# Performance work log

Hardware: AMD Instinct MI355X
Metric: run time of the kernel (lower is better)

Reference implementation:

```python
import jax, jax.numpy as jnp
import numpy as np


def setup_inputs() -> dict:
    key = jax.random.key(0)
    ks = jax.random.split(key, 8)
    n_src, n_dst, n_edges = 100000, 50000, 600000
    d_in, d_out = 128, 128
    n_reuse, n_cache = 5000, 8000
    full_dst_len = n_dst + n_reuse

    feat_src = jax.random.normal(ks[0], (n_src, d_in), jnp.float32)
    src = jax.random.randint(ks[1], (n_edges,), 0, n_src)
    dst = jax.random.randint(ks[2], (n_edges,), 0, n_dst)
    # xavier-ish init for the two bias-free Linear layers (stored as [out, in] like torch)
    W_self = jax.random.normal(ks[3], (d_out, d_in), jnp.float32) / np.sqrt(d_in).astype(np.float32)
    W_neigh = jax.random.normal(ks[4], (d_out, d_in), jnp.float32) / np.sqrt(d_in).astype(np.float32)
    # reuse_indices must be unique positions within [0, full_dst_len)
    reuse_indices = jnp.sort(jax.random.permutation(ks[5], full_dst_len)[:n_reuse])
    reuse_embedding = jax.random.normal(ks[6], (n_reuse, d_out), jnp.float32)
    cache_indices = jax.random.randint(ks[7], (n_cache,), 0, full_dst_len)
    return dict(feat_src=feat_src, W_self=W_self, W_neigh=W_neigh,
                reuse_embedding=reuse_embedding, src=src, dst=dst,
                reuse_indices=reuse_indices, cache_indices=cache_indices,
                n_dst=n_dst)


def reference(feat_src, W_self, W_neigh, reuse_embedding, src, dst,
              reuse_indices, cache_indices, n_dst):
    # --- GraphSAGE 'mean' aggregation on a block graph ---
    feat_dst = feat_src[:n_dst]                         # [n_dst, D_in]
    msgs = feat_src[src]                                # [E, D_in] copy_src gather
    ssum = jax.ops.segment_sum(msgs, dst, num_segments=n_dst)          # [n_dst, D_in]
    deg = jax.ops.segment_sum(jnp.ones_like(msgs[:, 0]), dst, num_segments=n_dst)
    h_neigh = jnp.where(deg[:, None] > 0, ssum / jnp.maximum(deg, 1.0)[:, None], 0.0)
    rst = feat_dst @ W_self.T + h_neigh @ W_neigh.T     # fc_self + fc_neigh

    # --- cache-reuse scatter merge (flag == 0 path) ---
    n_reuse = reuse_indices.shape[0]
    full_dst_len = n_dst + n_reuse
    keep = jnp.ones((full_dst_len,), dtype=bool).at[reuse_indices].set(False)
    unprune_indices = jnp.nonzero(keep, size=n_dst)[0]  # np.delete equivalent
    full = jnp.zeros((full_dst_len, rst.shape[1]), rst.dtype)
    full = full.at[unprune_indices].set(rst).at[reuse_indices].set(reuse_embedding)
    cache_embedding = jax.lax.stop_gradient(full[cache_indices])  # .detach()
    return full, cache_embedding
```

## Files before the change

kernel.cpp:

```cpp
#include <hip/hip_runtime.h>

#define N_DST   50000
#define D       128
#define MAXDEG  64

typedef __attribute__((ext_vector_type(8))) short bf16x8;
typedef __attribute__((ext_vector_type(4))) float f32x4;

__device__ __forceinline__ unsigned short f2bf(float f) {
    unsigned u = __float_as_uint(f);
    u += 0x7FFFu + ((u >> 16) & 1u);
    return (unsigned short)(u >> 16);
}

__global__ void build_ell_kernel(const int* __restrict__ src,
                                 const int* __restrict__ dst,
                                 int* __restrict__ ell,
                                 int* __restrict__ cnt,
                                 int n_edges) {
    int e = blockIdx.x * blockDim.x + threadIdx.x;
    if (e >= n_edges) return;
    int d = dst[e];
    int pos = atomicAdd(&cnt[d], 1);
    if (pos < MAXDEG)
        ell[(size_t)d * MAXDEG + pos] = src[e];
}

__global__ void rowpos_kernel(const int* __restrict__ reuse_idx,
                              int* __restrict__ rowpos, int n_reuse) {
    int i = blockIdx.x * blockDim.x + threadIdx.x;
    if (i >= N_DST) return;
    int lo = 0, hi = n_reuse;
    while (lo < hi) {
        int mid = (lo + hi) >> 1;
        if (reuse_idx[mid] - mid > i) hi = mid; else lo = mid + 1;
    }
    rowpos[i] = i + lo;
}

__global__ void wconv_kernel(const float* __restrict__ Wself,
                             const float* __restrict__ Wneigh,
                             unsigned short* __restrict__ wbf) {
    int idx = blockIdx.x * blockDim.x + threadIdx.x;
    if (idx >= 128 * 256) return;
    int n = idx >> 8;
    int k = idx & 255;
    float v = (k < 128) ? Wself[n * 128 + k] : Wneigh[n * 128 + (k - 128)];
    wbf[idx] = f2bf(v);
}

__global__ __launch_bounds__(256)
void gather_kernel(const float* __restrict__ feat,
                   const int* __restrict__ ell,
                   const int* __restrict__ cnt,
                   unsigned int* __restrict__ hneigh_u32) {
    int gid  = blockIdx.x * blockDim.x + threadIdx.x;
    int row  = gid >> 5;
    int lane = gid & 31;
    if (row >= N_DST) return;

    int deg = cnt[row];
    int n = min(deg, MAXDEG);
    float inv = 1.0f / fmaxf((float)deg, 1.0f);
    const int* rell = ell + (size_t)row * MAXDEG;

    float4 acc = make_float4(0.f, 0.f, 0.f, 0.f);
    int j = 0;
    for (; j + 4 <= n; j += 4) {
        int s0 = rell[j + 0];
        int s1 = rell[j + 1];
        int s2 = rell[j + 2];
        int s3 = rell[j + 3];
        float4 v0 = *(const float4*)&feat[(size_t)s0 * D + 4 * lane];
        float4 v1 = *(const float4*)&feat[(size_t)s1 * D + 4 * lane];
        float4 v2 = *(const float4*)&feat[(size_t)s2 * D + 4 * lane];
        float4 v3 = *(const float4*)&feat[(size_t)s3 * D + 4 * lane];
        acc.x += v0.x + v1.x + v2.x + v3.x;
        acc.y += v0.y + v1.y + v2.y + v3.y;
        acc.z += v0.z + v1.z + v2.z + v3.z;
        acc.w += v0.w + v1.w + v2.w + v3.w;
    }
    for (; j < n; ++j) {
        int s = rell[j];
        float4 v = *(const float4*)&feat[(size_t)s * D + 4 * lane];
        acc.x += v.x;
        acc.y += v.y;
        acc.z += v.z;
        acc.w += v.w;
    }
    unsigned p0 = (unsigned)f2bf(acc.x * inv) | ((unsigned)f2bf(acc.y * inv) << 16);
    unsigned p1 = (unsigned)f2bf(acc.z * inv) | ((unsigned)f2bf(acc.w * inv) << 16);
    uint2 out; out.x = p0; out.y = p1;
    *(uint2*)&hneigh_u32[(size_t)row * 64 + 2 * lane] = out;
}

__global__ __launch_bounds__(256, 2)
void gemm_kernel(const float* __restrict__ feat,
                 const unsigned short* __restrict__ hneigh,
                 const unsigned short* __restrict__ wbf,
                 const int* __restrict__ rowpos,
                 float* __restrict__ full) {
    __shared__ unsigned short Wl[128 * 256];

    int tid = threadIdx.x;
    {
        int n = tid >> 1;
        int ckbase = (tid & 1) * 16;
        const uint4* s = (const uint4*)(wbf + n * 256);
        uint4* d = (uint4*)(Wl + n * 256);
#pragma unroll
        for (int i = 0; i < 16; ++i) {
            int ck = ckbase + i;
            d[ck ^ (n & 7)] = s[ck];
        }
    }
    __syncthreads();

    int wv   = tid >> 6;
    int lane = tid & 63;
    int l15  = lane & 15;
    int q    = lane >> 4;
    int rowbase = blockIdx.x * 128 + wv * 32;

    f32x4 acc[2][8];
#pragma unroll
    for (int rt = 0; rt < 2; ++rt)
#pragma unroll
        for (int ct = 0; ct < 8; ++ct) acc[rt][ct] = (f32x4){0.f, 0.f, 0.f, 0.f};

    int r0c = min(rowbase + l15,      N_DST - 1);
    int r1c = min(rowbase + 16 + l15, N_DST - 1);

#pragma unroll 1
    for (int s = 0; s < 4; ++s) {
        int k0 = s * 32 + q * 8;
        float4 a0lo = *(const float4*)(feat + (size_t)r0c * D + k0);
        float4 a0hi = *(const float4*)(feat + (size_t)r0c * D + k0 + 4);
        float4 a1lo = *(const float4*)(feat + (size_t)r1c * D + k0);
        float4 a1hi = *(const float4*)(feat + (size_t)r1c * D + k0 + 4);
        union { bf16x8 v; unsigned short u[8]; } a0, a1;
        a0.u[0] = f2bf(a0lo.x); a0.u[1] = f2bf(a0lo.y);
        a0.u[2] = f2bf(a0lo.z); a0.u[3] = f2bf(a0lo.w);
        a0.u[4] = f2bf(a0hi.x); a0.u[5] = f2bf(a0hi.y);
        a0.u[6] = f2bf(a0hi.z); a0.u[7] = f2bf(a0hi.w);
        a1.u[0] = f2bf(a1lo.x); a1.u[1] = f2bf(a1lo.y);
        a1.u[2] = f2bf(a1lo.z); a1.u[3] = f2bf(a1lo.w);
        a1.u[4] = f2bf(a1hi.x); a1.u[5] = f2bf(a1hi.y);
        a1.u[6] = f2bf(a1hi.z); a1.u[7] = f2bf(a1hi.w);
#pragma unroll
        for (int ct = 0; ct < 8; ++ct) {
            int n = ct * 16 + l15;
            int ck = s * 4 + q;
            bf16x8 b = *(const bf16x8*)(Wl + n * 256 + ((ck ^ (n & 7)) << 3));
            acc[0][ct] = __builtin_amdgcn_mfma_f32_16x16x32_bf16(a0.v, b, acc[0][ct], 0, 0, 0);
            acc[1][ct] = __builtin_amdgcn_mfma_f32_16x16x32_bf16(a1.v, b, acc[1][ct], 0, 0, 0);
        }
    }
#pragma unroll 1
    for (int s = 0; s < 4; ++s) {
        int k0 = s * 32 + q * 8;
        bf16x8 a0 = *(const bf16x8*)(hneigh + (size_t)r0c * D + k0);
        bf16x8 a1 = *(const bf16x8*)(hneigh + (size_t)r1c * D + k0);
#pragma unroll
        for (int ct = 0; ct < 8; ++ct) {
            int n = ct * 16 + l15;
            int ck = 16 + s * 4 + q;
            bf16x8 b = *(const bf16x8*)(Wl + n * 256 + ((ck ^ (n & 7)) << 3));
            acc[0][ct] = __builtin_amdgcn_mfma_f32_16x16x32_bf16(a0, b, acc[0][ct], 0, 0, 0);
            acc[1][ct] = __builtin_amdgcn_mfma_f32_16x16x32_bf16(a1, b, acc[1][ct], 0, 0, 0);
        }
    }

#pragma unroll
    for (int rt = 0; rt < 2; ++rt) {
#pragma unroll
        for (int reg = 0; reg < 4; ++reg) {
            int gm = rowbase + rt * 16 + q * 4 + reg;
            if (gm < N_DST) {
                int jj = rowpos[gm];
                float* outr = full + (size_t)jj * D + l15;
#pragma unroll
                for (int ct = 0; ct < 8; ++ct)
                    outr[ct * 16] = acc[rt][ct][reg];
            }
        }
    }
}

__global__ void reuse_copy_kernel(const float* __restrict__ emb,
                                  const int* __restrict__ ridx,
                                  float* __restrict__ full, int n) {
    int idx = blockIdx.x * blockDim.x + threadIdx.x;
    int r = idx >> 5;
    if (r >= n) return;
    int c4 = (idx & 31) * 4;
    *(float4*)&full[ridx[r] * D + c4] = *(const float4*)&emb[r * D + c4];
}

__global__ void cache_gather_kernel(const float* __restrict__ full,
                                    const int* __restrict__ cidx,
                                    float* __restrict__ out, int n) {
    int idx = blockIdx.x * blockDim.x + threadIdx.x;
    int r = idx >> 5;
    if (r >= n) return;
    int c4 = (idx & 31) * 4;
    *(float4*)&out[r * D + c4] = *(const float4*)&full[cidx[r] * D + c4];
}

extern "C" void kernel_launch(void* const* d_in, const int* in_sizes, int n_in,
                              void* d_out, int out_size, void* d_ws, size_t ws_size,
                              hipStream_t stream) {
    const float* feat_src  = (const float*)d_in[0];
    const float* W_self    = (const float*)d_in[1];
    const float* W_neigh   = (const float*)d_in[2];
    const float* reuse_emb = (const float*)d_in[3];
    const int*   src       = (const int*)d_in[4];
    const int*   dst       = (const int*)d_in[5];
    const int*   reuse_idx = (const int*)d_in[6];
    const int*   cache_idx = (const int*)d_in[7];

    int n_edges = in_sizes[4];
    int n_reuse = in_sizes[6];
    int n_cache = in_sizes[7];
    int full_len = N_DST + n_reuse;

    unsigned short* hneigh = (unsigned short*)d_ws;
    int*   cnt    = (int*)(hneigh + (size_t)N_DST * D);
    int*   rowpos = cnt + N_DST;
    unsigned short* wbf = (unsigned short*)(rowpos + N_DST);

    float* full = (float*)d_out;
    float* cache_out = full + (size_t)full_len * D;

    int* ell = (int*)full;

    hipMemsetAsync(cnt, 0, (size_t)N_DST * sizeof(int), stream);

    build_ell_kernel<<<(n_edges + 255) / 256, 256, 0, stream>>>(
        src, dst, ell, cnt, n_edges);

    rowpos_kernel<<<(N_DST + 255) / 256, 256, 0, stream>>>(
        reuse_idx, rowpos, n_reuse);

    wconv_kernel<<<(128 * 256 + 255) / 256, 256, 0, stream>>>(
        W_self, W_neigh, wbf);

    gather_kernel<<<(N_DST * 32 + 255) / 256, 256, 0, stream>>>(
        feat_src, ell, cnt, (unsigned int*)hneigh);

    gemm_kernel<<<(N_DST + 127) / 128, 256, 0, stream>>>(
        feat_src, hneigh, wbf, rowpos, full);

    reuse_copy_kernel<<<(n_reuse * 32 + 255) / 256, 256, 0, stream>>>(
        reuse_emb, reuse_idx, full, n_reuse);

    cache_gather_kernel<<<(n_cache * 32 + 255) / 256, 256, 0, stream>>>(
        full, cache_idx, cache_out, n_cache);
}
```

Measured before the change: 201.5 us.

## Pre-convert source features to bf16 and gather from the bf16 copy

New measurement: 193.6 us. -3.9%, faster.

```diff
diff --git a/kernel.cpp b/kernel.cpp
--- a/kernel.cpp
+++ b/kernel.cpp
@@ -1,5 +1,6 @@
 #include <hip/hip_runtime.h>
 
+#define N_SRC   100000
 #define N_DST   50000
 #define D       128
 #define MAXDEG  64
@@ -11,6 +12,9 @@
     unsigned u = __float_as_uint(f);
     u += 0x7FFFu + ((u >> 16) & 1u);
     return (unsigned short)(u >> 16);
+}
+__device__ __forceinline__ float bf2f(unsigned short u) {
+    return __uint_as_float((unsigned)u << 16);
 }
 
 __global__ void build_ell_kernel(const int* __restrict__ src,
@@ -26,27 +30,90 @@
         ell[(size_t)d * MAXDEG + pos] = src[e];
 }
 
-__global__ void rowpos_kernel(const int* __restrict__ reuse_idx,
-                              int* __restrict__ rowpos, int n_reuse) {
+__global__ void aux_kernel(const int* __restrict__ reuse_idx,
+                           int* __restrict__ rowpos, int n_reuse,
+                           const float* __restrict__ Wself,
+                           const float* __restrict__ Wneigh,
+                           unsigned short* __restrict__ wbf) {
     int i = blockIdx.x * blockDim.x + threadIdx.x;
-    if (i >= N_DST) return;
-    int lo = 0, hi = n_reuse;
-    while (lo < hi) {
-        int mid = (lo + hi) >> 1;
-        if (reuse_idx[mid] - mid > i) hi = mid; else lo = mid + 1;
-    }
-    rowpos[i] = i + lo;
-}
-
-__global__ void wconv_kernel(const float* __restrict__ Wself,
-                             const float* __restrict__ Wneigh,
-                             unsigned short* __restrict__ wbf) {
-    int idx = blockIdx.x * blockDim.x + threadIdx.x;
-    if (idx >= 128 * 256) return;
-    int n = idx >> 8;
-    int k = idx & 255;
-    float v = (k < 128) ? Wself[n * 128 + k] : Wneigh[n * 128 + (k - 128)];
-    wbf[idx] = f2bf(v);
+    if (i < 128 * 256) {
+        int n = i >> 8;
+        int k = i & 255;
+        float v = (k < 128) ? Wself[n * 128 + k] : Wneigh[n * 128 + (k - 128)];
+        wbf[i] = f2bf(v);
+    }
+    if (i < N_DST) {
+        int lo = 0, hi = n_reuse;
+        while (lo < hi) {
+            int mid = (lo + hi) >> 1;
+            if (reuse_idx[mid] - mid > i) hi = mid; else lo = mid + 1;
+        }
+        rowpos[i] = i + lo;
+    }
+}
+
+__global__ __launch_bounds__(256)
+void featconv_kernel(const float* __restrict__ feat,
+                     unsigned int* __restrict__ featbf_u32,
+                     int n4) {
+    int stride = gridDim.x * blockDim.x;
+    for (int i = blockIdx.x * blockDim.x + threadIdx.x; i < n4; i += stride) {
+        float4 v = *(const float4*)(feat + (size_t)i * 4);
+        uint2 o;
+        o.x = (unsigned)f2bf(v.x) | ((unsigned)f2bf(v.y) << 16);
+        o.y = (unsigned)f2bf(v.z) | ((unsigned)f2bf(v.w) << 16);
+        *(uint2*)(featbf_u32 + (size_t)i * 2) = o;
+    }
+}
+
+__global__ __launch_bounds__(256)
+void gather_bf16_kernel(const unsigned short* __restrict__ featbf,
+                        const int* __restrict__ ell,
+                        const int* __restrict__ cnt,
+                        uint4* __restrict__ hneigh_u4) {
+    int gid  = blockIdx.x * blockDim.x + threadIdx.x;
+    int row  = gid >> 4;
+    int lane = gid & 15;
+    if (row >= N_DST) return;
+
+    int deg = cnt[row];
+    int n = min(deg, MAXDEG);
+    float inv = 1.0f / fmaxf((float)deg, 1.0f);
+    const int* rell = ell + (size_t)row * MAXDEG;
+
+    float acc[8];
+#pragma unroll
+    for (int k = 0; k < 8; ++k) acc[k] = 0.f;
+
+    union U { uint4 v; unsigned short us[8]; };
+    int j = 0;
+    for (; j + 4 <= n; j += 4) {
+        int s0 = rell[j + 0];
+        int s1 = rell[j + 1];
+        int s2 = rell[j + 2];
+        int s3 = rell[j + 3];
+        U a, b, c, d;
+        a.v = *(const uint4*)(featbf + (size_t)s0 * D + lane * 8);
+        b.v = *(const uint4*)(featbf + (size_t)s1 * D + lane * 8);
+        c.v = *(const uint4*)(featbf + (size_t)s2 * D + lane * 8);
+        d.v = *(const uint4*)(featbf + (size_t)s3 * D + lane * 8);
+#pragma unroll
+        for (int k = 0; k < 8; ++k)
+            acc[k] += (bf2f(a.us[k]) + bf2f(b.us[k])) + (bf2f(c.us[k]) + bf2f(d.us[k]));
+    }
+    for (; j < n; ++j) {
+        int s = rell[j];
+        U a;
+        a.v = *(const uint4*)(featbf + (size_t)s * D + lane * 8);
+#pragma unroll
+        for (int k = 0; k < 8; ++k) acc[k] += bf2f(a.us[k]);
+    }
+    uint4 o;
+    o.x = (unsigned)f2bf(acc[0] * inv) | ((unsigned)f2bf(acc[1] * inv) << 16);
+    o.y = (unsigned)f2bf(acc[2] * inv) | ((unsigned)f2bf(acc[3] * inv) << 16);
+    o.z = (unsigned)f2bf(acc[4] * inv) | ((unsigned)f2bf(acc[5] * inv) << 16);
+    o.w = (unsigned)f2bf(acc[6] * inv) | ((unsigned)f2bf(acc[7] * inv) << 16);
+    hneigh_u4[(size_t)row * 16 + lane] = o;
 }
 
 __global__ __launch_bounds__(256)
@@ -224,36 +291,68 @@
     int n_cache = in_sizes[7];
     int full_len = N_DST + n_reuse;
 
-    unsigned short* hneigh = (unsigned short*)d_ws;
-    int*   cnt    = (int*)(hneigh + (size_t)N_DST * D);
-    int*   rowpos = cnt + N_DST;
-    unsigned short* wbf = (unsigned short*)(rowpos + N_DST);
-
     float* full = (float*)d_out;
     float* cache_out = full + (size_t)full_len * D;
 
-    int* ell = (int*)full;
-
-    hipMemsetAsync(cnt, 0, (size_t)N_DST * sizeof(int), stream);
-
-    build_ell_kernel<<<(n_edges + 255) / 256, 256, 0, stream>>>(
-        src, dst, ell, cnt, n_edges);
-
-    rowpos_kernel<<<(N_DST + 255) / 256, 256, 0, stream>>>(
-        reuse_idx, rowpos, n_reuse);
-
-    wconv_kernel<<<(128 * 256 + 255) / 256, 256, 0, stream>>>(
-        W_self, W_neigh, wbf);
-
-    gather_kernel<<<(N_DST * 32 + 255) / 256, 256, 0, stream>>>(
-        feat_src, ell, cnt, (unsigned int*)hneigh);
-
-    gemm_kernel<<<(N_DST + 127) / 128, 256, 0, stream>>>(
-        feat_src, hneigh, wbf, rowpos, full);
-
-    reuse_copy_kernel<<<(n_reuse * 32 + 255) / 256, 256, 0, stream>>>(
-        reuse_emb, reuse_idx, full, n_reuse);
-
-    cache_gather_kernel<<<(n_cache * 32 + 255) / 256, 256, 0, stream>>>(
-        full, cache_idx, cache_out, n_cache);
-}
+    size_t hneigh_b = (size_t)N_DST * D * sizeof(unsigned short);
+    size_t ell_b    = (size_t)N_DST * MAXDEG * sizeof(int);
+    size_t need     = hneigh_b + ell_b + 2 * (size_t)N_DST * 4 + 128 * 256 * 2;
+
+    if (ws_size >= need) {
+        unsigned short* hneigh = (unsigned short*)d_ws;
+        int*   ell    = (int*)((char*)d_ws + hneigh_b);
+        int*   cnt    = (int*)((char*)ell + ell_b);
+        int*   rowpos = cnt + N_DST;
+        unsigned short* wbf = (unsigned short*)(rowpos + N_DST);
+        unsigned short* featbf = (unsigned short*)full;
+
+        hipMemsetAsync(cnt, 0, (size_t)N_DST * sizeof(int), stream);
+
+        build_ell_kernel<<<(n_edges + 255) / 256, 256, 0, stream>>>(
+            src, dst, ell, cnt, n_edges);
+
+        aux_kernel<<<(N_DST + 255) / 256, 256, 0, stream>>>(
+            reuse_idx, rowpos, n_reuse, W_self, W_neigh, wbf);
+
+        featconv_kernel<<<2048, 256, 0, stream>>>(
+            feat_src, (unsigned int*)featbf, N_SRC * (D / 4));
+
+        gather_bf16_kernel<<<(N_DST * 16 + 255) / 256, 256, 0, stream>>>(
+            featbf, ell, cnt, (uint4*)hneigh);
+
+        gemm_kernel<<<(N_DST + 127) / 128, 256, 0, stream>>>(
+            feat_src, hneigh, wbf, rowpos, full);
+
+        reuse_copy_kernel<<<(n_reuse * 32 + 255) / 256, 256, 0, stream>>>(
+            reuse_emb, reuse_idx, full, n_reuse);
+
+        cache_gather_kernel<<<(n_cache * 32 + 255) / 256, 256, 0, stream>>>(
+            full, cache_idx, cache_out, n_cache);
+    } else {
+        unsigned short* hneigh = (unsigned short*)d_ws;
+        int*   cnt    = (int*)(hneigh + (size_t)N_DST * D);
+        int*   rowpos = cnt + N_DST;
+        unsigned short* wbf = (unsigned short*)(rowpos + N_DST);
+        int* ell = (int*)full;
+
+        hipMemsetAsync(cnt, 0, (size_t)N_DST * sizeof(int), stream);
+
+        build_ell_kernel<<<(n_edges + 255) / 256, 256, 0, stream>>>(
+            src, dst, ell, cnt, n_edges);
+
+        aux_kernel<<<(N_DST + 255) / 256, 256, 0, stream>>>(
+            reuse_idx, rowpos, n_reuse, W_self, W_neigh, wbf);
+
+        gather_kernel<<<(N_DST * 32 + 255) / 256, 256, 0, stream>>>(
+            feat_src, ell, cnt, (unsigned int*)hneigh);
+
+        gemm_kernel<<<(N_DST + 127) / 128, 256, 0, stream>>>(
+            feat_src, hneigh, wbf, rowpos, full);
+
+        reuse_copy_kernel<<<(n_reuse * 32 + 255) / 256, 256, 0, stream>>>(
+            reuse_emb, reuse_idx, full, n_reuse);
+
+        cache_gather_kernel<<<(n_cache * 32 + 255) / 256, 256, 0, stream>>>(
+            full, cache_idx, cache_out, n_cache);
+    }
+}
```
